# Kernel optimization log

Hardware: AMD Instinct MI355X
Metric: run time of the kernel (lower is better)

Reference implementation:

```python
import jax, jax.numpy as jnp
import numpy as np

DIM = 1024
H = 16
D = DIM // H  # head_dim = 64
SCALE = 1.0 / (D ** 0.5 * 1.0)  # 1/(sqrt(head_dim)*temperature)
MIN_CUTOFF = 1e-15


def setup_inputs() -> dict:
    key = jax.random.key(0)
    ks = jax.random.split(key, 6)
    B, T = 2, 2048
    x = jax.random.normal(ks[0], (B, T, DIM), dtype=jnp.float32)
    cutoffs = jax.random.uniform(ks[1], (B, T, T), dtype=jnp.float32)
    # torch nn.Linear params: weight [out, in], bias [out]
    W_qkv = jax.random.normal(ks[2], (3 * DIM, DIM), dtype=jnp.float32) * (DIM ** -0.5)
    b_qkv = jax.random.normal(ks[3], (3 * DIM,), dtype=jnp.float32) * 0.01
    W_out = jax.random.normal(ks[4], (DIM, DIM), dtype=jnp.float32) * (DIM ** -0.5)
    b_out = jax.random.normal(ks[5], (DIM,), dtype=jnp.float32) * 0.01
    return {"x": x, "cutoffs": cutoffs, "W_qkv": W_qkv, "b_qkv": b_qkv,
            "W_out": W_out, "b_out": b_out}


def reference(x, cutoffs, W_qkv, b_qkv, W_out, b_out):
    B, T, _ = x.shape
    # QKV projection -> [B, T, 3, H, D] -> [3, B, H, T, D]
    qkv = (jnp.einsum('btc,oc->bto', x, W_qkv) + b_qkv)
    qkv = qkv.reshape(B, T, 3, H, D).transpose(2, 0, 3, 1, 4)
    q, k, v = qkv[0], qkv[1], qkv[2]
    # additive log-bias from cutoffs, broadcast over heads
    bias = jnp.log(jnp.clip(cutoffs, MIN_CUTOFF, None))[:, None, :, :]  # [B,1,T,T]
    scores = jnp.einsum('bhqd,bhkd->bhqk', q, k) * SCALE + bias
    attn = jax.nn.softmax(scores, axis=-1)
    out = jnp.einsum('bhqk,bhkd->bhqd', attn, v)  # [B,H,T,D]
    out = out.transpose(0, 2, 1, 3).reshape(B, T, DIM)
    return jnp.einsum('btc,oc->bto', out, W_out) + b_out
```

## Files before the change

### kernel.cpp

```cpp
#include <hip/hip_runtime.h>

typedef __attribute__((ext_vector_type(4))) float f32x4;
typedef __attribute__((ext_vector_type(8))) short bf16x8;

__device__ __forceinline__ unsigned short f2bf(float f) {
    union { float f; unsigned u; } v; v.f = f;
    unsigned r = v.u + 0x7FFFu + ((v.u >> 16) & 1u);
    return (unsigned short)(r >> 16);
}
__device__ __forceinline__ float bf2f(unsigned short s) {
    union { unsigned u; float f; } v; v.u = ((unsigned)s) << 16;
    return v.f;
}

#define GLD16(gp, lp)                                                          \
    __builtin_amdgcn_global_load_lds(                                          \
        (const __attribute__((address_space(1))) void*)(gp),                   \
        (__attribute__((address_space(3))) void*)(lp), 16, 0, 0)

__global__ void k_cvt(const float* __restrict__ in, unsigned short* __restrict__ out, int n4) {
    int i = blockIdx.x * blockDim.x + threadIdx.x;
    int stride = gridDim.x * blockDim.x;
    for (; i < n4; i += stride) {
        float4 v = reinterpret_cast<const float4*>(in)[i];
        ushort4 o;
        o.x = f2bf(v.x); o.y = f2bf(v.y); o.z = f2bf(v.z); o.w = f2bf(v.w);
        reinterpret_cast<ushort4*>(out)[i] = o;
    }
}

__global__ void k_cvtc(const float* __restrict__ in, unsigned short* __restrict__ out, int n4) {
    int i = blockIdx.x * blockDim.x + threadIdx.x;
    int stride = gridDim.x * blockDim.x;
    for (; i < n4; i += stride) {
        float4 v = reinterpret_cast<const float4*>(in)[i];
        ushort4 o;
        o.x = f2bf(fmaxf(v.x, 1e-15f)); o.y = f2bf(fmaxf(v.y, 1e-15f));
        o.z = f2bf(fmaxf(v.z, 1e-15f)); o.w = f2bf(fmaxf(v.w, 1e-15f));
        reinterpret_cast<ushort4*>(out)[i] = o;
    }
}

template <int MODE, int BM>
__global__ __launch_bounds__(256) void gemm_bt(
    const unsigned short* __restrict__ A, const unsigned short* __restrict__ B,
    const float* __restrict__ bias, float* __restrict__ outf,
    unsigned short* __restrict__ qb, unsigned short* __restrict__ kb,
    unsigned short* __restrict__ vb, int M, int N, int K)
{
    constexpr int FM = BM / 32;
    __shared__ unsigned short sA[2][BM * 32];
    __shared__ unsigned short sB[2][128 * 32];
    const int tid = threadIdx.x;
    const int w = tid >> 6, lane = tid & 63, g = lane >> 4, r = lane & 15;
    const int tm = blockIdx.x * BM, tn = blockIdx.y * 128;
    const int wr = w >> 1, wc = w & 1;

    f32x4 acc[FM][4];
#pragma unroll
    for (int i = 0; i < FM; i++)
#pragma unroll
        for (int j = 0; j < 4; j++) acc[i][j] = (f32x4)0.f;

    const unsigned short* ga0 = A + (size_t)(tm + w * (BM / 4) + (lane >> 2)) * K + (lane & 3) * 8;
    const unsigned short* gb0 = B + (size_t)(tn + w * 32 + (lane >> 2)) * K + (lane & 3) * 8;
    const int labase = w * (BM / 4) * 32;
    const int lbbase = w * 32 * 32;

    auto stageAB = [&](int nb, int kk) {
        GLD16(ga0 + kk, &sA[nb][labase]);
        if (BM == 128) GLD16(ga0 + kk + (size_t)16 * K, &sA[nb][labase + 16 * 32]);
        GLD16(gb0 + kk, &sB[nb][lbbase]);
        GLD16(gb0 + kk + (size_t)16 * K, &sB[nb][lbbase + 16 * 32]);
    };

    stageAB(0, 0);

    for (int kk = 0; kk < K; kk += 32) {
        const int cur = (kk >> 5) & 1;
        __syncthreads();
        if (kk + 32 < K) stageAB(cur ^ 1, kk + 32);
        bf16x8 af[FM], bfv[4];
#pragma unroll
        for (int f = 0; f < FM; f++)
            af[f] = *(const bf16x8*)&sA[cur][(wr * (BM / 2) + f * 16 + r) * 32 + g * 8];
#pragma unroll
        for (int f = 0; f < 4; f++)
            bfv[f] = *(const bf16x8*)&sB[cur][(wc * 64 + f * 16 + r) * 32 + g * 8];
        __builtin_amdgcn_s_setprio(1);
#pragma unroll
        for (int i = 0; i < FM; i++)
#pragma unroll
            for (int j = 0; j < 4; j++)
                acc[i][j] = __builtin_amdgcn_mfma_f32_16x16x32_bf16(af[i], bfv[j], acc[i][j], 0, 0, 0);
        __builtin_amdgcn_s_setprio(0);
    }

#pragma unroll
    for (int fj = 0; fj < 4; fj++) {
        int n = tn + wc * 64 + fj * 16 + r;
        float bn = bias[n];
#pragma unroll
        for (int fi = 0; fi < FM; fi++) {
#pragma unroll
            for (int j = 0; j < 4; j++) {
                int m = tm + wr * (BM / 2) + fi * 16 + 4 * g + j;
                float v = acc[fi][fj][j] + bn;
                if (MODE == 0) {
                    outf[(size_t)m * N + n] = v;
                } else {
                    int three = n >> 10, h = (n >> 6) & 15, d = n & 63;
                    int b = m >> 11, t = m & 2047, bh = b * 16 + h;
                    if (three == 0) {
                        qb[((size_t)bh * 2048 + t) * 64 + d] = f2bf(v * 0.18033688f);
                    } else if (three == 1) {
                        kb[((size_t)bh * 2048 + t) * 64 + d] = f2bf(v);
                    } else {
                        vb[((size_t)bh * 64 + d) * 2048 + t] = f2bf(v);
                    }
                }
            }
        }
    }
}

__global__ __launch_bounds__(256) void attn_kernel(
    const unsigned short* __restrict__ qbuf, const unsigned short* __restrict__ kbuf,
    const unsigned short* __restrict__ vbuf, const unsigned short* __restrict__ cutb,
    unsigned short* __restrict__ outa)
{
    __shared__ unsigned short sK[2][64 * 64], sV[2][64 * 64], sP[4][16 * 64];
    const int tid = threadIdx.x, w = tid >> 6, lane = tid & 63, g = lane >> 4, r = lane & 15;
    const int qt = blockIdx.x, h = blockIdx.y, b = blockIdx.z;
    const int q0 = qt * 64, bh = b * 16 + h;

    bf16x8 aq[2];
    {
        const unsigned short* qp = qbuf + ((size_t)bh * 2048 + q0 + w * 16 + r) * 64;
        aq[0] = *(const bf16x8*)(qp + g * 8);
        aq[1] = *(const bf16x8*)(qp + 32 + g * 8);
    }

    const int c = lane & 7, rr = lane >> 3;
    auto stage = [&](int nb, int kt) {
#pragma unroll
        for (int i = 0; i < 2; i++) {
            int row = w * 16 + i * 8 + rr;
            GLD16(kbuf + ((size_t)bh * 2048 + kt * 64 + row) * 64 + (c ^ (row & 7)) * 8,
                  &sK[nb][(w * 16 + i * 8) * 64]);
            GLD16(vbuf + ((size_t)bh * 64 + row) * 2048 + kt * 64 + (c ^ (row & 7)) * 8,
                  &sV[nb][(w * 16 + i * 8) * 64]);
        }
    };

    const unsigned short* cp[4];
#pragma unroll
    for (int j = 0; j < 4; j++)
        cp[j] = cutb + ((size_t)b * 2048 + (q0 + w * 16 + 4 * g + j)) * 2048 + r;

    f32x4 oacc[4];
#pragma unroll
    for (int f = 0; f < 4; f++) oacc[f] = (f32x4)0.f;
    float psum[4] = {0.f, 0.f, 0.f, 0.f};

    unsigned short* sPw = sP[w];

    stage(0, 0);

    for (int kt = 0; kt < 32; kt++) {
        const int cur = kt & 1;
        __syncthreads();
        if (kt < 31) stage(cur ^ 1, kt + 1);

        unsigned short cu[4][4];
#pragma unroll
        for (int f = 0; f < 4; f++)
#pragma unroll
            for (int j = 0; j < 4; j++) cu[f][j] = cp[j][kt * 64 + f * 16];

        f32x4 sa[4];
#pragma unroll
        for (int f = 0; f < 4; f++) sa[f] = (f32x4)0.f;
        __builtin_amdgcn_s_setprio(1);
#pragma unroll
        for (int s = 0; s < 2; s++)
#pragma unroll
            for (int f = 0; f < 4; f++) {
                int krow = f * 16 + r;
                bf16x8 bk = *(const bf16x8*)&sK[cur][krow * 64 + ((s * 32 + g * 8) ^ ((krow & 7) << 3))];
                sa[f] = __builtin_amdgcn_mfma_f32_16x16x32_bf16(aq[s], bk, sa[f], 0, 0, 0);
            }
        __builtin_amdgcn_s_setprio(0);

#pragma unroll
        for (int f = 0; f < 4; f++)
#pragma unroll
            for (int j = 0; j < 4; j++) {
                float p = bf2f(cu[f][j]) * exp2f(sa[f][j]);
                psum[j] += p;
                int row = 4 * g + j, col = f * 16 + r;
                sPw[row * 64 + (col ^ ((row & 7) << 3))] = f2bf(p);
            }

        __builtin_amdgcn_s_setprio(1);
#pragma unroll
        for (int s = 0; s < 2; s++) {
            bf16x8 pa = *(const bf16x8*)&sPw[r * 64 + ((s * 32 + g * 8) ^ ((r & 7) << 3))];
#pragma unroll
            for (int f = 0; f < 4; f++) {
                int drow = f * 16 + r;
                bf16x8 bvv = *(const bf16x8*)&sV[cur][drow * 64 + ((s * 32 + g * 8) ^ ((drow & 7) << 3))];
                oacc[f] = __builtin_amdgcn_mfma_f32_16x16x32_bf16(pa, bvv, oacc[f], 0, 0, 0);
            }
        }
        __builtin_amdgcn_s_setprio(0);
    }

#pragma unroll
    for (int j = 0; j < 4; j++) {
        psum[j] += __shfl_xor(psum[j], 1);
        psum[j] += __shfl_xor(psum[j], 2);
        psum[j] += __shfl_xor(psum[j], 4);
        psum[j] += __shfl_xor(psum[j], 8);
    }

#pragma unroll
    for (int j = 0; j < 4; j++) {
        float inv = 1.f / psum[j];
        int q = q0 + w * 16 + 4 * g + j;
#pragma unroll
        for (int f = 0; f < 4; f++) {
            int d = f * 16 + r;
            outa[((size_t)(b * 2048 + q)) * 1024 + h * 64 + d] = f2bf(oacc[f][j] * inv);
        }
    }
}

extern "C" void kernel_launch(void* const* d_in, const int* in_sizes, int n_in,
                              void* d_out, int out_size, void* d_ws, size_t ws_size,
                              hipStream_t stream) {
    const float* x       = (const float*)d_in[0];
    const float* cutoffs = (const float*)d_in[1];
    const float* Wqkv    = (const float*)d_in[2];
    const float* bqkv    = (const float*)d_in[3];
    const float* Wout    = (const float*)d_in[4];
    const float* bout    = (const float*)d_in[5];
    float* out = (float*)d_out;

    char* ws = (char*)d_ws;
    unsigned short* x_bf    = (unsigned short*)ws;  ws += (size_t)4096 * 1024 * 2;
    unsigned short* wqkv_bf = (unsigned short*)ws;  ws += (size_t)3072 * 1024 * 2;
    unsigned short* wout_bf = (unsigned short*)ws;  ws += (size_t)1024 * 1024 * 2;
    unsigned short* qb      = (unsigned short*)ws;  ws += (size_t)32 * 2048 * 64 * 2;
    unsigned short* kb      = (unsigned short*)ws;  ws += (size_t)32 * 2048 * 64 * 2;
    unsigned short* vb      = (unsigned short*)ws;  ws += (size_t)32 * 2048 * 64 * 2;
    unsigned short* attn_o  = (unsigned short*)ws;  ws += (size_t)4096 * 1024 * 2;
    unsigned short* cutb    = (unsigned short*)ws;  ws += (size_t)2 * 2048 * 2048 * 2;

    k_cvt<<<1024, 256, 0, stream>>>(x,    x_bf,    4096 * 1024 / 4);
    k_cvt<<<1024, 256, 0, stream>>>(Wqkv, wqkv_bf, 3072 * 1024 / 4);
    k_cvt<<<512,  256, 0, stream>>>(Wout, wout_bf, 1024 * 1024 / 4);
    k_cvtc<<<2048, 256, 0, stream>>>(cutoffs, cutb, 2 * 2048 * 2048 / 4);

    gemm_bt<1, 128><<<dim3(32, 24), 256, 0, stream>>>(x_bf, wqkv_bf, bqkv, nullptr,
                                                      qb, kb, vb, 4096, 3072, 1024);
    attn_kernel<<<dim3(32, 16, 2), 256, 0, stream>>>(qb, kb, vb, cutb, attn_o);
    gemm_bt<0, 64><<<dim3(64, 8), 256, 0, stream>>>(attn_o, wout_bf, bout, out,
                                                    nullptr, nullptr, nullptr, 4096, 1024, 1024);
}
```

Measured before the change: 270.6 us.

## Transpose score MFMA for vector cutoff loads, single-buffer K/V staging

In the attention kernel the QK^T MFMA operands are swapped so each lane owns one query row and four consecutive keys. This allows cutoff values to be read as ushort4 vectors, P to be packed with v_cvt_pk_bf16_f32 and stored as 8-byte writes, and the row sum to be kept as one scalar reduced across lane groups. K/V staging drops double buffering in favour of load-then-sync each iteration, which removes the prefetch overlap and may expose load latency. The GEMM loop moves its barrier to the end of the iteration, drops s_setprio and adds unroll 2.

New measurement: 257.1 us. 5.0% less time.

```diff
diff --git a/kernel.cpp b/kernel.cpp
--- a/kernel.cpp
+++ b/kernel.cpp
@@ -75,10 +75,11 @@
     };
 
     stageAB(0, 0);
-
+    __syncthreads();
+
+#pragma unroll 2
     for (int kk = 0; kk < K; kk += 32) {
         const int cur = (kk >> 5) & 1;
-        __syncthreads();
         if (kk + 32 < K) stageAB(cur ^ 1, kk + 32);
         bf16x8 af[FM], bfv[4];
 #pragma unroll
@@ -87,13 +88,12 @@
 #pragma unroll
         for (int f = 0; f < 4; f++)
             bfv[f] = *(const bf16x8*)&sB[cur][(wc * 64 + f * 16 + r) * 32 + g * 8];
-        __builtin_amdgcn_s_setprio(1);
 #pragma unroll
         for (int i = 0; i < FM; i++)
 #pragma unroll
             for (int j = 0; j < 4; j++)
                 acc[i][j] = __builtin_amdgcn_mfma_f32_16x16x32_bf16(af[i], bfv[j], acc[i][j], 0, 0, 0);
-        __builtin_amdgcn_s_setprio(0);
+        __syncthreads();
     }
 
 #pragma unroll
@@ -129,7 +129,7 @@
     const unsigned short* __restrict__ vbuf, const unsigned short* __restrict__ cutb,
     unsigned short* __restrict__ outa)
 {
-    __shared__ unsigned short sK[2][64 * 64], sV[2][64 * 64], sP[4][16 * 64];
+    __shared__ unsigned short sK[64 * 64], sV[64 * 64], sP[4][16 * 64];
     const int tid = threadIdx.x, w = tid >> 6, lane = tid & 63, g = lane >> 4, r = lane & 15;
     const int qt = blockIdx.x, h = blockIdx.y, b = blockIdx.z;
     const int q0 = qt * 64, bh = b * 16 + h;
@@ -142,41 +142,36 @@
     }
 
     const int c = lane & 7, rr = lane >> 3;
-    auto stage = [&](int nb, int kt) {
+    auto stage = [&](int kt) {
 #pragma unroll
         for (int i = 0; i < 2; i++) {
             int row = w * 16 + i * 8 + rr;
             GLD16(kbuf + ((size_t)bh * 2048 + kt * 64 + row) * 64 + (c ^ (row & 7)) * 8,
-                  &sK[nb][(w * 16 + i * 8) * 64]);
+                  sK + (w * 16 + i * 8) * 64);
             GLD16(vbuf + ((size_t)bh * 64 + row) * 2048 + kt * 64 + (c ^ (row & 7)) * 8,
-                  &sV[nb][(w * 16 + i * 8) * 64]);
+                  sV + (w * 16 + i * 8) * 64);
         }
     };
 
-    const unsigned short* cp[4];
-#pragma unroll
-    for (int j = 0; j < 4; j++)
-        cp[j] = cutb + ((size_t)b * 2048 + (q0 + w * 16 + 4 * g + j)) * 2048 + r;
+    const unsigned short* cq = cutb + ((size_t)b * 2048 + (q0 + w * 16 + r)) * 2048 + 4 * g;
 
     f32x4 oacc[4];
 #pragma unroll
     for (int f = 0; f < 4; f++) oacc[f] = (f32x4)0.f;
-    float psum[4] = {0.f, 0.f, 0.f, 0.f};
+    float psum = 0.f;
 
     unsigned short* sPw = sP[w];
-
-    stage(0, 0);
+    const int pswz = (r & 7) << 3;
 
     for (int kt = 0; kt < 32; kt++) {
-        const int cur = kt & 1;
         __syncthreads();
-        if (kt < 31) stage(cur ^ 1, kt + 1);
-
-        unsigned short cu[4][4];
+        stage(kt);
+
+        ushort4 cf[4];
 #pragma unroll
         for (int f = 0; f < 4; f++)
-#pragma unroll
-            for (int j = 0; j < 4; j++) cu[f][j] = cp[j][kt * 64 + f * 16];
+            cf[f] = *(const ushort4*)(cq + kt * 64 + 16 * f);
+        __syncthreads();
 
         f32x4 sa[4];
 #pragma unroll
@@ -187,46 +182,54 @@
 #pragma unroll
             for (int f = 0; f < 4; f++) {
                 int krow = f * 16 + r;
-                bf16x8 bk = *(const bf16x8*)&sK[cur][krow * 64 + ((s * 32 + g * 8) ^ ((krow & 7) << 3))];
-                sa[f] = __builtin_amdgcn_mfma_f32_16x16x32_bf16(aq[s], bk, sa[f], 0, 0, 0);
+                bf16x8 bk = *(const bf16x8*)&sK[krow * 64 + ((s * 32 + g * 8) ^ ((krow & 7) << 3))];
+                sa[f] = __builtin_amdgcn_mfma_f32_16x16x32_bf16(bk, aq[s], sa[f], 0, 0, 0);
             }
         __builtin_amdgcn_s_setprio(0);
 
-#pragma unroll
-        for (int f = 0; f < 4; f++)
-#pragma unroll
-            for (int j = 0; j < 4; j++) {
-                float p = bf2f(cu[f][j]) * exp2f(sa[f][j]);
-                psum[j] += p;
-                int row = 4 * g + j, col = f * 16 + r;
-                sPw[row * 64 + (col ^ ((row & 7) << 3))] = f2bf(p);
-            }
+        float p[4][4];
+#pragma unroll
+        for (int f = 0; f < 4; f++) {
+            p[f][0] = bf2f(cf[f].x) * exp2f(sa[f][0]);
+            p[f][1] = bf2f(cf[f].y) * exp2f(sa[f][1]);
+            p[f][2] = bf2f(cf[f].z) * exp2f(sa[f][2]);
+            p[f][3] = bf2f(cf[f].w) * exp2f(sa[f][3]);
+        }
+        psum += (((p[0][0] + p[0][1]) + (p[0][2] + p[0][3])) +
+                 ((p[1][0] + p[1][1]) + (p[1][2] + p[1][3]))) +
+                (((p[2][0] + p[2][1]) + (p[2][2] + p[2][3])) +
+                 ((p[3][0] + p[3][1]) + (p[3][2] + p[3][3])));
+
+#pragma unroll
+        for (int f = 0; f < 4; f++) {
+            unsigned pk0, pk1;
+            asm("v_cvt_pk_bf16_f32 %0, %1, %2" : "=v"(pk0) : "v"(p[f][0]), "v"(p[f][1]));
+            asm("v_cvt_pk_bf16_f32 %0, %1, %2" : "=v"(pk1) : "v"(p[f][2]), "v"(p[f][3]));
+            int col = (16 * f + 4 * g) ^ pswz;
+            uint2 pr; pr.x = pk0; pr.y = pk1;
+            *reinterpret_cast<uint2*>(&sPw[r * 64 + col]) = pr;
+        }
 
         __builtin_amdgcn_s_setprio(1);
 #pragma unroll
         for (int s = 0; s < 2; s++) {
-            bf16x8 pa = *(const bf16x8*)&sPw[r * 64 + ((s * 32 + g * 8) ^ ((r & 7) << 3))];
+            bf16x8 pa = *(const bf16x8*)&sPw[r * 64 + ((s * 32 + g * 8) ^ pswz)];
 #pragma unroll
             for (int f = 0; f < 4; f++) {
                 int drow = f * 16 + r;
-                bf16x8 bvv = *(const bf16x8*)&sV[cur][drow * 64 + ((s * 32 + g * 8) ^ ((drow & 7) << 3))];
+                bf16x8 bvv = *(const bf16x8*)&sV[drow * 64 + ((s * 32 + g * 8) ^ ((drow & 7) << 3))];
                 oacc[f] = __builtin_amdgcn_mfma_f32_16x16x32_bf16(pa, bvv, oacc[f], 0, 0, 0);
             }
         }
         __builtin_amdgcn_s_setprio(0);
     }
 
+    psum += __shfl_xor(psum, 16);
+    psum += __shfl_xor(psum, 32);
+
 #pragma unroll
     for (int j = 0; j < 4; j++) {
-        psum[j] += __shfl_xor(psum[j], 1);
-        psum[j] += __shfl_xor(psum[j], 2);
-        psum[j] += __shfl_xor(psum[j], 4);
-        psum[j] += __shfl_xor(psum[j], 8);
-    }
-
-#pragma unroll
-    for (int j = 0; j < 4; j++) {
-        float inv = 1.f / psum[j];
+        float inv = 1.f / __shfl(psum, 4 * g + j);
         int q = q0 + w * 16 + 4 * g + j;
 #pragma unroll
         for (int f = 0; f < 4; f++) {
```
